# Performance work log

Hardware: AMD Instinct MI355X
Metric: run time of the kernel (lower is better)

## Reference

```python
import jax, jax.numpy as jnp
import numpy as np

B, S, E, H = 2, 2048, 1024, 16
HD = E // H


def setup_inputs() -> dict:
    key = jax.random.key(0)
    ks = jax.random.split(key, 5)
    scale = 0.02
    return {
        "x": jax.random.normal(ks[0], (B, S, E), dtype=jnp.float32),
        "qkv_w": jax.random.normal(ks[1], (3 * E, E), dtype=jnp.float32) * scale,
        "qkv_b": jax.random.normal(ks[2], (3 * E,), dtype=jnp.float32) * scale,
        "out_w": jax.random.normal(ks[3], (E, E), dtype=jnp.float32) * scale,
        "out_b": jax.random.normal(ks[4], (E,), dtype=jnp.float32) * scale,
    }


def reference(x, qkv_w, qkv_b, out_w, out_b):
    b, s, e = x.shape
    scale = 1.0 / jnp.sqrt(jnp.float32(HD))
    # fused QKV projection: torch Linear is x @ W.T + b
    qkv = x @ qkv_w.T + qkv_b                       # [b, s, 3e]
    qkv = qkv.reshape(b, s, 3, H, HD)
    qkv = jnp.transpose(qkv, (2, 0, 3, 1, 4))       # [3, b, h, s, hd]
    q, k, v = qkv[0], qkv[1], qkv[2]
    scores = jnp.einsum('bhqd,bhkd->bhqk', q, k) * scale
    # causal mask (atmask=True): mask strictly upper triangle
    causal = jnp.triu(jnp.ones((s, s), dtype=bool), k=1)
    scores = jnp.where(causal, -jnp.inf, scores)
    attn = jax.nn.softmax(scores, axis=-1)          # dropout p=0.0 -> identity
    out = jnp.einsum('bhqk,bhkd->bhqd', attn, v)    # [b, h, s, hd]
    out = jnp.transpose(out, (0, 2, 1, 3)).reshape(b, s, e)
    return out @ out_w.T + out_b
```

## Files before the change

### kernel.cpp

```cpp
#include <hip/hip_runtime.h>
#include <cmath>

typedef __attribute__((ext_vector_type(8))) __bf16 bf16x8;
typedef __attribute__((ext_vector_type(4))) float f32x4;

__device__ inline unsigned short f2bf(float f) {
    unsigned int u = __float_as_uint(f);
    unsigned int r = (u + 0x7fffu + ((u >> 16) & 1u)) >> 16;
    return (unsigned short)r;
}

__device__ inline bf16x8 ld8(const unsigned short* p) {
    uint4 v = *(const uint4*)p;
    return __builtin_bit_cast(bf16x8, v);
}

__device__ inline f32x4 mfma16(bf16x8 a, bf16x8 b, f32x4 c) {
    return __builtin_amdgcn_mfma_f32_16x16x32_bf16(a, b, c, 0, 0, 0);
}

__device__ inline unsigned pk2(float a, float b) {
    return ((__float_as_uint(a) + 0x8000u) >> 16) |
           ((__float_as_uint(b) + 0x8000u) & 0xffff0000u);
}

__device__ inline void store_out(float* C, size_t idx, float v) { C[idx] = v; }
__device__ inline void store_out(unsigned short* C, size_t idx, float v) { C[idx] = f2bf(v); }

__device__ inline void gl_lds16(const unsigned short* g, unsigned short* l) {
    __builtin_amdgcn_global_load_lds(
        (const __attribute__((address_space(1))) void*)(unsigned long long)g,
        (__attribute__((address_space(3))) void*)(unsigned)(unsigned long long)l,
        16, 0, 0);
}

#define NX4  1048576
#define NW14 786432
#define NW24 262144
__global__ __launch_bounds__(256) void cvt3(const float* __restrict__ x,
                                            const float* __restrict__ w1,
                                            const float* __restrict__ w2,
                                            unsigned short* __restrict__ xb,
                                            unsigned short* __restrict__ w1b,
                                            unsigned short* __restrict__ w2b) {
    int i = blockIdx.x * 256 + threadIdx.x;
    const float* src;
    unsigned short* dst;
    int off;
    if (i < NX4)              { src = x;  dst = xb;  off = i; }
    else if (i < NX4 + NW14)  { src = w1; dst = w1b; off = i - NX4; }
    else                      { src = w2; dst = w2b; off = i - NX4 - NW14; }
    float4 v = ((const float4*)src)[off];
    ushort4 o;
    o.x = f2bf(v.x); o.y = f2bf(v.y); o.z = f2bf(v.z); o.w = f2bf(v.w);
    ((ushort4*)dst)[off] = o;
}

template <typename OutT>
__global__ __launch_bounds__(256) void gemm_bt(const unsigned short* __restrict__ A,
                                               const unsigned short* __restrict__ B,
                                               const float* __restrict__ bias,
                                               OutT* __restrict__ C,
                                               int M, int N, int K) {
    __shared__ __align__(16) unsigned short As[128 * 32];
    __shared__ __align__(16) unsigned short Bs[128 * 32];
    const int m0 = blockIdx.y * 128;
    const int n0 = blockIdx.x * 128;
    const int t = threadIdx.x;
    const int wave = t >> 6, lane = t & 63;
    const int l16 = lane & 15, quad = lane >> 4;
    const int wm = (wave >> 1) * 64, wn = (wave & 1) * 64;

    f32x4 acc[4][4] = {};

    const int c0 = t, c1 = 256 + t;
    const int r0 = c0 >> 2, kc0 = (c0 & 3) * 8;
    const int r1 = c1 >> 2, kc1 = (c1 & 3) * 8;

    for (int k0 = 0; k0 < K; k0 += 32) {
        __syncthreads();
        gl_lds16(A + (size_t)(m0 + r0) * K + k0 + kc0, As + c0 * 8);
        gl_lds16(B + (size_t)(n0 + r0) * K + k0 + kc0, Bs + c0 * 8);
        gl_lds16(A + (size_t)(m0 + r1) * K + k0 + kc1, As + c1 * 8);
        gl_lds16(B + (size_t)(n0 + r1) * K + k0 + kc1, Bs + c1 * 8);
        __syncthreads();

        bf16x8 af[4], bfr[4];
        #pragma unroll
        for (int i = 0; i < 4; ++i)
            af[i] = ld8(As + (wm + i * 16 + l16) * 32 + quad * 8);
        #pragma unroll
        for (int j = 0; j < 4; ++j)
            bfr[j] = ld8(Bs + (wn + j * 16 + l16) * 32 + quad * 8);
        #pragma unroll
        for (int i = 0; i < 4; ++i)
            #pragma unroll
            for (int j = 0; j < 4; ++j)
                acc[i][j] = mfma16(af[i], bfr[j], acc[i][j]);
    }

    #pragma unroll
    for (int i = 0; i < 4; ++i) {
        #pragma unroll
        for (int j = 0; j < 4; ++j) {
            int col = n0 + wn + j * 16 + l16;
            float bv = bias[col];
            #pragma unroll
            for (int r = 0; r < 4; ++r) {
                int row = m0 + wm + i * 16 + quad * 4 + r;
                store_out(C, (size_t)row * N + col, acc[i][j][r] + bv);
            }
        }
    }
}

__global__ __launch_bounds__(256) void pack_kv(const unsigned short* __restrict__ qkv,
                                               unsigned short* __restrict__ kvp) {
    const int S = 2048, E = 1024, LD = 3072;
    const int tile = blockIdx.x;
    const int bh = blockIdx.y;
    const int b = bh >> 4, h = bh & 15;
    const int t = threadIdx.x;
    __shared__ __align__(16) unsigned short Kt[32][64];
    __shared__ __align__(16) unsigned short Vt[32][64];
    const size_t gbase = (size_t)b * S * LD + h * 64;
    const unsigned short* Kg = qkv + gbase + E;
    const unsigned short* Vg = qkv + gbase + 2 * E;
    {
        int key = t >> 3, j = (t & 7) * 8;
        size_t off = (size_t)(tile * 32 + key) * LD + j;
        *(uint4*)&Kt[key][j] = *(const uint4*)(Kg + off);
        *(uint4*)&Vt[key][j] = *(const uint4*)(Vg + off);
    }
    __syncthreads();
    unsigned short* dst = kvp + ((size_t)bh * 64 + tile) * 4096;
    {
        int f = t >> 6, lane = t & 63;
        int l16 = lane & 15, quad = lane >> 4;
        int key = 8 * (l16 >> 2) + (l16 & 3) + ((f & 2) ? 4 : 0);
        int hdo = (f & 1) * 32 + quad * 8;
        *(uint4*)(dst + f * 512 + lane * 8) = *(const uint4*)&Kt[key][hdo];
        int hd = f * 16 + l16;
        unsigned short tmp[8];
        #pragma unroll
        for (int jj = 0; jj < 8; ++jj) tmp[jj] = Vt[quad * 8 + jj][hd];
        *(uint4*)(dst + 2048 + f * 512 + lane * 8) = *(uint4*)tmp;
    }
}

__global__ __launch_bounds__(256, 4) void attn_kernel(const unsigned short* __restrict__ qkv,
                                                      const unsigned short* __restrict__ kvp,
                                                      unsigned short* __restrict__ out) {
    const int S = 2048, E = 1024, LD = 3072;
    const int wavei = threadIdx.x >> 6;
    const int lane = threadIdx.x & 63;
    const int l16 = lane & 15, quad = lane >> 4;
    const int pairIdx = blockIdx.x;
    const int bh = pairIdx & 31;
    const int qtile = 127 - (pairIdx >> 5);
    const int b = bh >> 4, h = bh & 15;
    const int q0 = qtile * 16;
    const int q = q0 + l16;
    const size_t base = (size_t)b * S * LD;
    const unsigned short* Qp = qkv + base + h * 64;

    bf16x8 bq0 = ld8(Qp + (size_t)(q0 + l16) * LD + quad * 8);
    bf16x8 bq1 = ld8(Qp + (size_t)(q0 + l16) * LD + 32 + quad * 8);

    const unsigned short* tbase = kvp + (size_t)bh * 64 * 4096;
    const int nchunks = (q0 + 79) >> 6;
    const int loff = lane * 8;

    f32x4 O[4] = {};
    float lsum = 0.f;
    const float scale = 0.125f;

    for (int c = wavei; c < nchunks; c += 4) {
        const unsigned short* tb0 = tbase + (size_t)(2 * c) * 4096;
        const unsigned short* tb1 = tb0 + 4096;
        bf16x8 a00 = ld8(tb0 + loff);
        bf16x8 a01 = ld8(tb0 + 512 + loff);
        bf16x8 a10 = ld8(tb0 + 1024 + loff);
        bf16x8 a11 = ld8(tb0 + 1536 + loff);
        bf16x8 w0  = ld8(tb0 + 2048 + loff);
        bf16x8 w1  = ld8(tb0 + 2560 + loff);
        bf16x8 w2  = ld8(tb0 + 3072 + loff);
        bf16x8 w3  = ld8(tb0 + 3584 + loff);
        bf16x8 e00 = ld8(tb1 + loff);
        bf16x8 e01 = ld8(tb1 + 512 + loff);
        bf16x8 e10 = ld8(tb1 + 1024 + loff);
        bf16x8 e11 = ld8(tb1 + 1536 + loff);
        bf16x8 x0  = ld8(tb1 + 2048 + loff);
        bf16x8 x1  = ld8(tb1 + 2560 + loff);
        bf16x8 x2  = ld8(tb1 + 3072 + loff);
        bf16x8 x3  = ld8(tb1 + 3584 + loff);

        const bool lastc = (c == nchunks - 1);
        const int ks = c * 64;

        {
            f32x4 s0 = {}, s1 = {};
            s0 = mfma16(a00, bq0, s0);
            s0 = mfma16(a01, bq1, s0);
            s1 = mfma16(a10, bq0, s1);
            s1 = mfma16(a11, bq1, s1);
            float p0[4], p1[4];
            if (lastc) {
                #pragma unroll
                for (int r = 0; r < 4; ++r) {
                    int kk = ks + quad * 8 + r;
                    p0[r] = (kk > q)     ? 0.f : __expf(s0[r] * scale);
                    p1[r] = (kk + 4 > q) ? 0.f : __expf(s1[r] * scale);
                }
            } else {
                #pragma unroll
                for (int r = 0; r < 4; ++r) {
                    p0[r] = __expf(s0[r] * scale);
                    p1[r] = __expf(s1[r] * scale);
                }
            }
            #pragma unroll
            for (int r = 0; r < 4; ++r) lsum += p0[r] + p1[r];
            uint4 pw;
            pw.x = pk2(p0[0], p0[1]);
            pw.y = pk2(p0[2], p0[3]);
            pw.z = pk2(p1[0], p1[1]);
            pw.w = pk2(p1[2], p1[3]);
            bf16x8 bpv = __builtin_bit_cast(bf16x8, pw);
            O[0] = mfma16(w0, bpv, O[0]);
            O[1] = mfma16(w1, bpv, O[1]);
            O[2] = mfma16(w2, bpv, O[2]);
            O[3] = mfma16(w3, bpv, O[3]);
        }

        if (!(lastc && (ks + 32 > q0 + 15))) {
            f32x4 s0 = {}, s1 = {};
            s0 = mfma16(e00, bq0, s0);
            s0 = mfma16(e01, bq1, s0);
            s1 = mfma16(e10, bq0, s1);
            s1 = mfma16(e11, bq1, s1);
            float p0[4], p1[4];
            if (lastc) {
                #pragma unroll
                for (int r = 0; r < 4; ++r) {
                    int kk = ks + 32 + quad * 8 + r;
                    p0[r] = (kk > q)     ? 0.f : __expf(s0[r] * scale);
                    p1[r] = (kk + 4 > q) ? 0.f : __expf(s1[r] * scale);
                }
            } else {
                #pragma unroll
                for (int r = 0; r < 4; ++r) {
                    p0[r] = __expf(s0[r] * scale);
                    p1[r] = __expf(s1[r] * scale);
                }
            }
            #pragma unroll
            for (int r = 0; r < 4; ++r) lsum += p0[r] + p1[r];
            uint4 pw;
            pw.x = pk2(p0[0], p0[1]);
            pw.y = pk2(p0[2], p0[3]);
            pw.z = pk2(p1[0], p1[1]);
            pw.w = pk2(p1[2], p1[3]);
            bf16x8 bpv = __builtin_bit_cast(bf16x8, pw);
            O[0] = mfma16(x0, bpv, O[0]);
            O[1] = mfma16(x1, bpv, O[1]);
            O[2] = mfma16(x2, bpv, O[2]);
            O[3] = mfma16(x3, bpv, O[3]);
        }
    }

    lsum += __shfl_xor(lsum, 16);
    lsum += __shfl_xor(lsum, 32);

    __shared__ float Ob[4][16][66];
    __shared__ float Lb[4][16];
    #pragma unroll
    for (int tn = 0; tn < 4; ++tn)
        #pragma unroll
        for (int r = 0; r < 4; ++r)
            Ob[wavei][l16][tn * 16 + quad * 4 + r] = O[tn][r];
    if (quad == 0) Lb[wavei][l16] = lsum;
    __syncthreads();

    const int t = threadIdx.x;
    const int qi = t >> 4, hdg = (t & 15) * 4;
    float ls = Lb[0][qi] + Lb[1][qi] + Lb[2][qi] + Lb[3][qi];
    float acc[4] = {0.f, 0.f, 0.f, 0.f};
    #pragma unroll
    for (int w = 0; w < 4; ++w)
        #pragma unroll
        for (int k = 0; k < 4; ++k)
            acc[k] += Ob[w][qi][hdg + k];
    const float invl = 1.0f / ls;
    ushort4 o;
    o.x = f2bf(acc[0] * invl);
    o.y = f2bf(acc[1] * invl);
    o.z = f2bf(acc[2] * invl);
    o.w = f2bf(acc[3] * invl);
    *(ushort4*)(out + (size_t)(b * S + q0 + qi) * E + h * 64 + hdg) = o;
}

extern "C" void kernel_launch(void* const* d_in, const int* in_sizes, int n_in,
                              void* d_out, int out_size, void* d_ws, size_t ws_size,
                              hipStream_t stream) {
    const float* x     = (const float*)d_in[0];
    const float* qkv_w = (const float*)d_in[1];
    const float* qkv_b = (const float*)d_in[2];
    const float* out_w = (const float*)d_in[3];
    const float* out_b = (const float*)d_in[4];
    float* out = (float*)d_out;

    const int B = 2, S = 2048, E = 1024;
    const int M = B * S;
    const int N1 = 3 * E;

    unsigned short* ws    = (unsigned short*)d_ws;
    unsigned short* xb    = ws;
    unsigned short* w1b   = xb + (size_t)M * E;
    unsigned short* kvp   = ws;
    unsigned short* w2b   = ws + (size_t)8 * 1024 * 1024;
    unsigned short* qkvb  = w2b + (size_t)E * E;
    unsigned short* attnb = qkvb + (size_t)M * N1;

    cvt3<<<dim3(8192), dim3(256), 0, stream>>>(x, qkv_w, out_w, xb, w1b, w2b);

    gemm_bt<unsigned short><<<dim3(N1 / 128, M / 128), dim3(256), 0, stream>>>(
        xb, w1b, qkv_b, qkvb, M, N1, E);

    pack_kv<<<dim3(64, 32), dim3(256), 0, stream>>>(qkvb, kvp);

    attn_kernel<<<dim3(4096), dim3(256), 0, stream>>>(qkvb, kvp, attnb);

    gemm_bt<float><<<dim3(E / 128, M / 128), dim3(256), 0, stream>>>(
        attnb, w2b, out_b, out, M, E, E);
}
```

Measured before the change: 196.6 us.

## Fuse KV packing into QKV GEMM epilogue and process two query tiles per block

The QKV GEMM now writes Q (pre-scaled by 1/sqrt(hd)) and K/V straight into MFMA-fragment layouts, which removes the separate pack_kv kernel and the round trip through the intermediate qkv buffer. The attention kernel handles 32 queries per block with two Q tiles sharing each K/V fragment load, which halves K/V traffic per query. The row sum is computed with an MFMA against a ones vector instead of scalar adds, and bf16 packing uses a byte-permute (truncation) instead of rounding. The costs are scattered 2-byte epilogue stores, higher register pressure (launch bounds drop to 3 blocks), and slightly different rounding.

```diff
diff --git a/kernel.cpp b/kernel.cpp
--- a/kernel.cpp
+++ b/kernel.cpp
@@ -2,6 +2,7 @@
 #include <cmath>
 
 typedef __attribute__((ext_vector_type(8))) __bf16 bf16x8;
+typedef __attribute__((ext_vector_type(8))) unsigned short ushort8v;
 typedef __attribute__((ext_vector_type(4))) float f32x4;
 
 __device__ inline unsigned short f2bf(float f) {
@@ -19,9 +20,8 @@
     return __builtin_amdgcn_mfma_f32_16x16x32_bf16(a, b, c, 0, 0, 0);
 }
 
-__device__ inline unsigned pk2(float a, float b) {
-    return ((__float_as_uint(a) + 0x8000u) >> 16) |
-           ((__float_as_uint(b) + 0x8000u) & 0xffff0000u);
+__device__ inline unsigned pk2t(float a, float b) {
+    return __builtin_amdgcn_perm(__float_as_uint(b), __float_as_uint(a), 0x07060302u);
 }
 
 __device__ inline void store_out(float* C, size_t idx, float v) { C[idx] = v; }
@@ -114,190 +114,240 @@
     }
 }
 
-__global__ __launch_bounds__(256) void pack_kv(const unsigned short* __restrict__ qkv,
-                                               unsigned short* __restrict__ kvp) {
-    const int S = 2048, E = 1024, LD = 3072;
-    const int tile = blockIdx.x;
-    const int bh = blockIdx.y;
-    const int b = bh >> 4, h = bh & 15;
+__global__ __launch_bounds__(256) void gemm_qkv(const unsigned short* __restrict__ A,
+                                                const unsigned short* __restrict__ B,
+                                                const float* __restrict__ bias,
+                                                unsigned short* __restrict__ qp,
+                                                unsigned short* __restrict__ kvp,
+                                                int M, int N, int K) {
+    __shared__ __align__(16) unsigned short As[128 * 32];
+    __shared__ __align__(16) unsigned short Bs[128 * 32];
+    const int m0 = blockIdx.y * 128;
+    const int n0 = blockIdx.x * 128;
     const int t = threadIdx.x;
-    __shared__ __align__(16) unsigned short Kt[32][64];
-    __shared__ __align__(16) unsigned short Vt[32][64];
-    const size_t gbase = (size_t)b * S * LD + h * 64;
-    const unsigned short* Kg = qkv + gbase + E;
-    const unsigned short* Vg = qkv + gbase + 2 * E;
-    {
-        int key = t >> 3, j = (t & 7) * 8;
-        size_t off = (size_t)(tile * 32 + key) * LD + j;
-        *(uint4*)&Kt[key][j] = *(const uint4*)(Kg + off);
-        *(uint4*)&Vt[key][j] = *(const uint4*)(Vg + off);
-    }
-    __syncthreads();
-    unsigned short* dst = kvp + ((size_t)bh * 64 + tile) * 4096;
-    {
-        int f = t >> 6, lane = t & 63;
-        int l16 = lane & 15, quad = lane >> 4;
-        int key = 8 * (l16 >> 2) + (l16 & 3) + ((f & 2) ? 4 : 0);
-        int hdo = (f & 1) * 32 + quad * 8;
-        *(uint4*)(dst + f * 512 + lane * 8) = *(const uint4*)&Kt[key][hdo];
-        int hd = f * 16 + l16;
-        unsigned short tmp[8];
-        #pragma unroll
-        for (int jj = 0; jj < 8; ++jj) tmp[jj] = Vt[quad * 8 + jj][hd];
-        *(uint4*)(dst + 2048 + f * 512 + lane * 8) = *(uint4*)tmp;
-    }
-}
-
-__global__ __launch_bounds__(256, 4) void attn_kernel(const unsigned short* __restrict__ qkv,
+    const int wave = t >> 6, lane = t & 63;
+    const int l16 = lane & 15, quad = lane >> 4;
+    const int wm = (wave >> 1) * 64, wn = (wave & 1) * 64;
+
+    f32x4 acc[4][4] = {};
+
+    const int c0 = t, c1 = 256 + t;
+    const int r0 = c0 >> 2, kc0 = (c0 & 3) * 8;
+    const int r1 = c1 >> 2, kc1 = (c1 & 3) * 8;
+
+    for (int k0 = 0; k0 < K; k0 += 32) {
+        __syncthreads();
+        gl_lds16(A + (size_t)(m0 + r0) * K + k0 + kc0, As + c0 * 8);
+        gl_lds16(B + (size_t)(n0 + r0) * K + k0 + kc0, Bs + c0 * 8);
+        gl_lds16(A + (size_t)(m0 + r1) * K + k0 + kc1, As + c1 * 8);
+        gl_lds16(B + (size_t)(n0 + r1) * K + k0 + kc1, Bs + c1 * 8);
+        __syncthreads();
+
+        bf16x8 af[4], bfr[4];
+        #pragma unroll
+        for (int i = 0; i < 4; ++i)
+            af[i] = ld8(As + (wm + i * 16 + l16) * 32 + quad * 8);
+        #pragma unroll
+        for (int j = 0; j < 4; ++j)
+            bfr[j] = ld8(Bs + (wn + j * 16 + l16) * 32 + quad * 8);
+        #pragma unroll
+        for (int i = 0; i < 4; ++i)
+            #pragma unroll
+            for (int j = 0; j < 4; ++j)
+                acc[i][j] = mfma16(af[i], bfr[j], acc[i][j]);
+    }
+
+    const int b = (m0 >> 11);
+    if (n0 < 1024) {
+        #pragma unroll
+        for (int j = 0; j < 4; ++j) {
+            int col = n0 + wn + j * 16 + l16;
+            float bv = bias[col];
+            int d = col & 63, hloc = col >> 6;
+            int half = d >> 5, qd = d & 31;
+            int lanep = (qd >> 3) * 16;
+            #pragma unroll
+            for (int i = 0; i < 4; ++i)
+                #pragma unroll
+                for (int r = 0; r < 4; ++r) {
+                    int s = (m0 + wm + i * 16 + quad * 4 + r) & 2047;
+                    int bh = b * 16 + hloc;
+                    int qt = s >> 4, q16 = s & 15;
+                    size_t pos = ((size_t)(bh * 128 + qt) * 2 + half) * 512 +
+                                 (lanep + q16) * 8 + (qd & 7);
+                    qp[pos] = f2bf((acc[i][j][r] + bv) * 0.125f);
+                }
+        }
+    } else if (n0 < 2048) {
+        #pragma unroll
+        for (int j = 0; j < 4; ++j) {
+            int col = n0 + wn + j * 16 + l16;
+            float bv = bias[col];
+            int d = col & 63, hloc = (col & 1023) >> 6;
+            int fbit0 = d >> 5, qd = d & 31;
+            int quadp = qd >> 3, elem = qd & 7;
+            #pragma unroll
+            for (int i = 0; i < 4; ++i)
+                #pragma unroll
+                for (int r = 0; r < 4; ++r) {
+                    int s = (m0 + wm + i * 16 + quad * 4 + r) & 2047;
+                    int bh = b * 16 + hloc;
+                    int tile = s >> 5, key = s & 31;
+                    int f = (((key & 7) >= 4) ? 2 : 0) | fbit0;
+                    int l16k = 4 * (key >> 3) + (key & 3);
+                    size_t pos = ((size_t)(bh * 64 + tile)) * 4096 + f * 512 +
+                                 (quadp * 16 + l16k) * 8 + elem;
+                    kvp[pos] = f2bf(acc[i][j][r] + bv);
+                }
+        }
+    } else {
+        #pragma unroll
+        for (int j = 0; j < 4; ++j) {
+            int col = n0 + wn + j * 16 + l16;
+            float bv = bias[col];
+            int d = col & 63, hloc = (col & 1023) >> 6;
+            int tn = d >> 4, l16v = d & 15;
+            #pragma unroll
+            for (int i = 0; i < 4; ++i)
+                #pragma unroll
+                for (int r = 0; r < 4; ++r) {
+                    int s = (m0 + wm + i * 16 + quad * 4 + r) & 2047;
+                    int bh = b * 16 + hloc;
+                    int tile = s >> 5, key = s & 31;
+                    size_t pos = ((size_t)(bh * 64 + tile)) * 4096 + 2048 + tn * 512 +
+                                 ((key >> 3) * 16 + l16v) * 8 + (key & 7);
+                    kvp[pos] = f2bf(acc[i][j][r] + bv);
+                }
+        }
+    }
+}
+
+__global__ __launch_bounds__(256, 3) void attn_kernel(const unsigned short* __restrict__ qp,
                                                       const unsigned short* __restrict__ kvp,
                                                       unsigned short* __restrict__ out) {
-    const int S = 2048, E = 1024, LD = 3072;
+    const int S = 2048, E = 1024;
     const int wavei = threadIdx.x >> 6;
     const int lane = threadIdx.x & 63;
     const int l16 = lane & 15, quad = lane >> 4;
-    const int pairIdx = blockIdx.x;
-    const int bh = pairIdx & 31;
-    const int qtile = 127 - (pairIdx >> 5);
+    const int bh = blockIdx.x & 31;
+    const int P = 63 - (int)(blockIdx.x >> 5);
     const int b = bh >> 4, h = bh & 15;
-    const int q0 = qtile * 16;
-    const int q = q0 + l16;
-    const size_t base = (size_t)b * S * LD;
-    const unsigned short* Qp = qkv + base + h * 64;
-
-    bf16x8 bq0 = ld8(Qp + (size_t)(q0 + l16) * LD + quad * 8);
-    bf16x8 bq1 = ld8(Qp + (size_t)(q0 + l16) * LD + 32 + quad * 8);
-
+    const int loff = lane * 8;
+
+    const unsigned short* qbase = qp + ((size_t)(bh * 128 + 2 * P) * 2) * 512;
+    bf16x8 bqA0 = ld8(qbase + loff);
+    bf16x8 bqA1 = ld8(qbase + 512 + loff);
+    bf16x8 bqB0 = ld8(qbase + 1024 + loff);
+    bf16x8 bqB1 = ld8(qbase + 1536 + loff);
+
+    ushort8v ov;
+    #pragma unroll
+    for (int j = 0; j < 8; ++j) ov[j] = 0x3F80;
+    const bf16x8 ones = __builtin_bit_cast(bf16x8, ov);
+
+    f32x4 OA[4] = {}, OB[4] = {};
+    f32x4 LA = {}, LB = {};
+    const int qA = 32 * P + l16, qB = qA + 16;
+    const int nchunks = (P + 2) >> 1;
     const unsigned short* tbase = kvp + (size_t)bh * 64 * 4096;
-    const int nchunks = (q0 + 79) >> 6;
-    const int loff = lane * 8;
-
-    f32x4 O[4] = {};
-    float lsum = 0.f;
-    const float scale = 0.125f;
 
     for (int c = wavei; c < nchunks; c += 4) {
-        const unsigned short* tb0 = tbase + (size_t)(2 * c) * 4096;
-        const unsigned short* tb1 = tb0 + 4096;
-        bf16x8 a00 = ld8(tb0 + loff);
-        bf16x8 a01 = ld8(tb0 + 512 + loff);
-        bf16x8 a10 = ld8(tb0 + 1024 + loff);
-        bf16x8 a11 = ld8(tb0 + 1536 + loff);
-        bf16x8 w0  = ld8(tb0 + 2048 + loff);
-        bf16x8 w1  = ld8(tb0 + 2560 + loff);
-        bf16x8 w2  = ld8(tb0 + 3072 + loff);
-        bf16x8 w3  = ld8(tb0 + 3584 + loff);
-        bf16x8 e00 = ld8(tb1 + loff);
-        bf16x8 e01 = ld8(tb1 + 512 + loff);
-        bf16x8 e10 = ld8(tb1 + 1024 + loff);
-        bf16x8 e11 = ld8(tb1 + 1536 + loff);
-        bf16x8 x0  = ld8(tb1 + 2048 + loff);
-        bf16x8 x1  = ld8(tb1 + 2560 + loff);
-        bf16x8 x2  = ld8(tb1 + 3072 + loff);
-        bf16x8 x3  = ld8(tb1 + 3584 + loff);
+        const unsigned short* tb = tbase + (size_t)c * 8192;
+        bf16x8 f[16];
+        #pragma unroll
+        for (int i = 0; i < 16; ++i) f[i] = ld8(tb + i * 512 + loff);
 
         const bool lastc = (c == nchunks - 1);
         const int ks = c * 64;
-
-        {
-            f32x4 s0 = {}, s1 = {};
-            s0 = mfma16(a00, bq0, s0);
-            s0 = mfma16(a01, bq1, s0);
-            s1 = mfma16(a10, bq0, s1);
-            s1 = mfma16(a11, bq1, s1);
-            float p0[4], p1[4];
+        const bool skip1 = lastc && ((P & 1) == 0);
+
+        #pragma unroll
+        for (int tile = 0; tile < 2; ++tile) {
+            if (tile == 1 && skip1) break;
+            const bf16x8* g = f + tile * 8;
+            const int kst = ks + tile * 32;
+
+            f32x4 sA0 = {}, sA1 = {}, sB0 = {}, sB1 = {};
+            sA0 = mfma16(g[0], bqA0, sA0);
+            sA0 = mfma16(g[1], bqA1, sA0);
+            sA1 = mfma16(g[2], bqA0, sA1);
+            sA1 = mfma16(g[3], bqA1, sA1);
+            sB0 = mfma16(g[0], bqB0, sB0);
+            sB0 = mfma16(g[1], bqB1, sB0);
+            sB1 = mfma16(g[2], bqB0, sB1);
+            sB1 = mfma16(g[3], bqB1, sB1);
+
+            float pA0[4], pA1[4], pB0[4], pB1[4];
             if (lastc) {
                 #pragma unroll
                 for (int r = 0; r < 4; ++r) {
-                    int kk = ks + quad * 8 + r;
-                    p0[r] = (kk > q)     ? 0.f : __expf(s0[r] * scale);
-                    p1[r] = (kk + 4 > q) ? 0.f : __expf(s1[r] * scale);
+                    int kk = kst + quad * 8 + r;
+                    pA0[r] = (kk > qA)     ? 0.f : __expf(sA0[r]);
+                    pA1[r] = (kk + 4 > qA) ? 0.f : __expf(sA1[r]);
+                    pB0[r] = (kk > qB)     ? 0.f : __expf(sB0[r]);
+                    pB1[r] = (kk + 4 > qB) ? 0.f : __expf(sB1[r]);
                 }
             } else {
                 #pragma unroll
                 for (int r = 0; r < 4; ++r) {
-                    p0[r] = __expf(s0[r] * scale);
-                    p1[r] = __expf(s1[r] * scale);
+                    pA0[r] = __expf(sA0[r]);
+                    pA1[r] = __expf(sA1[r]);
+                    pB0[r] = __expf(sB0[r]);
+                    pB1[r] = __expf(sB1[r]);
                 }
             }
-            #pragma unroll
-            for (int r = 0; r < 4; ++r) lsum += p0[r] + p1[r];
-            uint4 pw;
-            pw.x = pk2(p0[0], p0[1]);
-            pw.y = pk2(p0[2], p0[3]);
-            pw.z = pk2(p1[0], p1[1]);
-            pw.w = pk2(p1[2], p1[3]);
-            bf16x8 bpv = __builtin_bit_cast(bf16x8, pw);
-            O[0] = mfma16(w0, bpv, O[0]);
-            O[1] = mfma16(w1, bpv, O[1]);
-            O[2] = mfma16(w2, bpv, O[2]);
-            O[3] = mfma16(w3, bpv, O[3]);
-        }
-
-        if (!(lastc && (ks + 32 > q0 + 15))) {
-            f32x4 s0 = {}, s1 = {};
-            s0 = mfma16(e00, bq0, s0);
-            s0 = mfma16(e01, bq1, s0);
-            s1 = mfma16(e10, bq0, s1);
-            s1 = mfma16(e11, bq1, s1);
-            float p0[4], p1[4];
-            if (lastc) {
-                #pragma unroll
-                for (int r = 0; r < 4; ++r) {
-                    int kk = ks + 32 + quad * 8 + r;
-                    p0[r] = (kk > q)     ? 0.f : __expf(s0[r] * scale);
-                    p1[r] = (kk + 4 > q) ? 0.f : __expf(s1[r] * scale);
-                }
-            } else {
-                #pragma unroll
-                for (int r = 0; r < 4; ++r) {
-                    p0[r] = __expf(s0[r] * scale);
-                    p1[r] = __expf(s1[r] * scale);
-                }
-            }
-            #pragma unroll
-            for (int r = 0; r < 4; ++r) lsum += p0[r] + p1[r];
-            uint4 pw;
-            pw.x = pk2(p0[0], p0[1]);
-            pw.y = pk2(p0[2], p0[3]);
-            pw.z = pk2(p1[0], p1[1]);
-            pw.w = pk2(p1[2], p1[3]);
-            bf16x8 bpv = __builtin_bit_cast(bf16x8, pw);
-            O[0] = mfma16(x0, bpv, O[0]);
-            O[1] = mfma16(x1, bpv, O[1]);
-            O[2] = mfma16(x2, bpv, O[2]);
-            O[3] = mfma16(x3, bpv, O[3]);
-        }
-    }
-
-    lsum += __shfl_xor(lsum, 16);
-    lsum += __shfl_xor(lsum, 32);
-
-    __shared__ float Ob[4][16][66];
-    __shared__ float Lb[4][16];
+            uint4 pwA, pwB;
+            pwA.x = pk2t(pA0[0], pA0[1]);
+            pwA.y = pk2t(pA0[2], pA0[3]);
+            pwA.z = pk2t(pA1[0], pA1[1]);
+            pwA.w = pk2t(pA1[2], pA1[3]);
+            pwB.x = pk2t(pB0[0], pB0[1]);
+            pwB.y = pk2t(pB0[2], pB0[3]);
+            pwB.z = pk2t(pB1[0], pB1[1]);
+            pwB.w = pk2t(pB1[2], pB1[3]);
+            bf16x8 bpA = __builtin_bit_cast(bf16x8, pwA);
+            bf16x8 bpB = __builtin_bit_cast(bf16x8, pwB);
+
+            OA[0] = mfma16(g[4], bpA, OA[0]);
+            OA[1] = mfma16(g[5], bpA, OA[1]);
+            OA[2] = mfma16(g[6], bpA, OA[2]);
+            OA[3] = mfma16(g[7], bpA, OA[3]);
+            LA    = mfma16(ones, bpA, LA);
+            OB[0] = mfma16(g[4], bpB, OB[0]);
+            OB[1] = mfma16(g[5], bpB, OB[1]);
+            OB[2] = mfma16(g[6], bpB, OB[2]);
+            OB[3] = mfma16(g[7], bpB, OB[3]);
+            LB    = mfma16(ones, bpB, LB);
+        }
+    }
+
+    __shared__ float Ob[4][32][66];
+    __shared__ float Lb[4][32];
     #pragma unroll
     for (int tn = 0; tn < 4; ++tn)
         #pragma unroll
-        for (int r = 0; r < 4; ++r)
-            Ob[wavei][l16][tn * 16 + quad * 4 + r] = O[tn][r];
-    if (quad == 0) Lb[wavei][l16] = lsum;
+        for (int r = 0; r < 4; ++r) {
+            Ob[wavei][l16][tn * 16 + quad * 4 + r]      = OA[tn][r];
+            Ob[wavei][16 + l16][tn * 16 + quad * 4 + r] = OB[tn][r];
+        }
+    if (quad == 0) {
+        Lb[wavei][l16]      = LA[0];
+        Lb[wavei][16 + l16] = LB[0];
+    }
     __syncthreads();
 
     const int t = threadIdx.x;
-    const int qi = t >> 4, hdg = (t & 15) * 4;
+    const int qi = t >> 3, hd0 = (t & 7) * 8;
     float ls = Lb[0][qi] + Lb[1][qi] + Lb[2][qi] + Lb[3][qi];
-    float acc[4] = {0.f, 0.f, 0.f, 0.f};
+    const float invl = 1.0f / ls;
+    unsigned short o[8];
     #pragma unroll
-    for (int w = 0; w < 4; ++w)
-        #pragma unroll
-        for (int k = 0; k < 4; ++k)
-            acc[k] += Ob[w][qi][hdg + k];
-    const float invl = 1.0f / ls;
-    ushort4 o;
-    o.x = f2bf(acc[0] * invl);
-    o.y = f2bf(acc[1] * invl);
-    o.z = f2bf(acc[2] * invl);
-    o.w = f2bf(acc[3] * invl);
-    *(ushort4*)(out + (size_t)(b * S + q0 + qi) * E + h * 64 + hdg) = o;
+    for (int k = 0; k < 8; ++k) {
+        float a = Ob[0][qi][hd0 + k] + Ob[1][qi][hd0 + k] +
+                  Ob[2][qi][hd0 + k] + Ob[3][qi][hd0 + k];
+        o[k] = f2bf(a * invl);
+    }
+    *(uint4*)(out + (size_t)(b * S + 32 * P + qi) * E + h * 64 + hd0) = *(uint4*)o;
 }
 
 extern "C" void kernel_launch(void* const* d_in, const int* in_sizes, int n_in,
@@ -316,20 +366,18 @@
 
     unsigned short* ws    = (unsigned short*)d_ws;
     unsigned short* xb    = ws;
-    unsigned short* w1b   = xb + (size_t)M * E;
-    unsigned short* kvp   = ws;
-    unsigned short* w2b   = ws + (size_t)8 * 1024 * 1024;
-    unsigned short* qkvb  = w2b + (size_t)E * E;
-    unsigned short* attnb = qkvb + (size_t)M * N1;
+    unsigned short* w1b   = xb   + (size_t)M * E;
+    unsigned short* w2b   = w1b  + (size_t)N1 * E;
+    unsigned short* qpb   = w2b  + (size_t)E * E;
+    unsigned short* kvpb  = qpb  + (size_t)32 * 128 * 1024;
+    unsigned short* attnb = kvpb + (size_t)32 * 64 * 4096;
 
     cvt3<<<dim3(8192), dim3(256), 0, stream>>>(x, qkv_w, out_w, xb, w1b, w2b);
 
-    gemm_bt<unsigned short><<<dim3(N1 / 128, M / 128), dim3(256), 0, stream>>>(
-        xb, w1b, qkv_b, qkvb, M, N1, E);
-
-    pack_kv<<<dim3(64, 32), dim3(256), 0, stream>>>(qkvb, kvp);
-
-    attn_kernel<<<dim3(4096), dim3(256), 0, stream>>>(qkvb, kvp, attnb);
+    gemm_qkv<<<dim3(N1 / 128, M / 128), dim3(256), 0, stream>>>(
+        xb, w1b, qkv_b, qpb, kvpb, M, N1, E);
+
+    attn_kernel<<<dim3(2048), dim3(256), 0, stream>>>(qpb, kvpb, attnb);
 
     gemm_bt<float><<<dim3(E / 128, M / 128), dim3(256), 0, stream>>>(
         attnb, w2b, out_b, out, M, E, E);
```

Result: faster. 188.8 us (-3.9%).
